# Kernel tuning notes

Measured on AMD Instinct MI355X. Metric: run time of the kernel, lower is better.

The kernel has to match this reference:

```python
import jax, jax.numpy as jnp
from jax import lax
import numpy as np

H, W = 4096, 4096
KERNEL_SIZES = [3, 5, 7, 9, 11, 13, 15]


def setup_inputs() -> dict:
    key = jax.random.key(0)
    k1, k2 = jax.random.split(key)
    x = jax.random.uniform(k1, (H, W), dtype=jnp.float32)
    base_map = jax.random.uniform(k2, (H, W), dtype=jnp.float32)
    return {"x": x, "base_map": base_map}


def _box_blur(x4, k):
    # replicate ('edge') padding by k//2, then VALID conv with uniform 1/k^2 kernel
    p = k // 2
    xp = jnp.pad(x4, ((0, 0), (0, 0), (p, p), (p, p)), mode='edge')
    w = jnp.full((1, 1, k, k), 1.0 / (k * k), dtype=x4.dtype)
    return lax.conv_general_dilated(
        xp, w, window_strides=(1, 1), padding='VALID',
        dimension_numbers=('NCHW', 'OIHW', 'NCHW'))


def reference(x, base_map):
    # x: [H, W] -> [1, 1, H, W]
    x4 = x[None, None, :, :]
    acc = jnp.zeros_like(x4)
    for k in KERNEL_SIZES:  # fixed small set of structurally distinct convs
        acc = acc + _box_blur(x4, k)
    out = (acc / len(KERNEL_SIZES)) * base_map[None, None, :, :]
    return out  # [1, 1, H, W]
```

## Files before the change

### kernel.cpp

```cpp
#include <hip/hip_runtime.h>

typedef __attribute__((ext_vector_type(2))) float f32x2;

#define W 4096
#define H 4096
#define NT 256
#define COLS 512
#define SR 32
#define GROUP 4
#define NSTAGE (SR + 14)
#define NG 12
#define LW 576
#define RAD 7
#define PEND 18

__device__ __forceinline__ void gl_lds16(float* lds, const float* g) {
    __builtin_amdgcn_global_load_lds(
        (const __attribute__((address_space(1))) void*)g,
        (__attribute__((address_space(3))) void*)lds, 16, 0, 0);
}
__device__ __forceinline__ void gl_lds4(float* lds, const float* g) {
    __builtin_amdgcn_global_load_lds(
        (const __attribute__((address_space(1))) void*)g,
        (__attribute__((address_space(3))) void*)lds, 4, 0, 0);
}

__global__ __launch_bounds__(NT, 4) void multibox_kernel(
    const float* __restrict__ x, const float* __restrict__ base,
    float* __restrict__ out)
{
    __shared__ float buf[3][GROUP][LW];

    const int t  = threadIdx.x;
    const int w  = t >> 6;
    const int l  = t & 63;
    const int c0 = blockIdx.x * COLS;
    const int i0 = blockIdx.y * SR;

    const float w3  = 1.f/(7.f*9.f);
    const float w5  = 1.f/(7.f*25.f);
    const float w7  = 1.f/(7.f*49.f);
    const float w9  = 1.f/(7.f*81.f);
    const float w11 = 1.f/(7.f*121.f);
    const float w13 = 1.f/(7.f*169.f);
    const float w15 = 1.f/(7.f*225.f);

    const int colL  = min(max(c0 -   8 +     l, 0), W - 1);
    const int colM1 =         c0 +  56 + 4 * l;
    const int colM2 =         c0 + 312 + 4 * l;
    const int colR  = min(    c0 + 504 +     l,     W - 1);

    auto stage = [&](int g, int b) {
        const int rc = min(max(i0 - RAD + g * GROUP + w, 0), H - 1);
        const float* rp = x + (size_t)rc * W;
        float* lb = &buf[b][w][0];
        gl_lds4 (lb,        rp + colL);
        gl_lds16(lb +  64,  rp + colM1);
        if (l < 48) gl_lds16(lb + 320, rp + colM2);
        gl_lds4 (lb + 512,  rp + colR);
    };

    f32x2 Pnd[PEND];
#pragma unroll
    for (int q = 0; q < PEND; ++q) Pnd[q] = f32x2{0.f, 0.f};

    auto compute_group = [&](int b, int g) {
#pragma unroll
        for (int rr = 0; rr < GROUP; ++rr) {
            if (g * GROUP + rr < NSTAGE) {
                const float* p = &buf[b][rr][2 * t];
                f32x2 q2[9];
#pragma unroll
                for (int i = 0; i < 9; ++i) q2[i] = *(const f32x2*)(p + 2 * i);

                auto PR = [&](int a) -> f32x2 {
                    if ((a & 1) == 0) return q2[a / 2];
                    f32x2 r;
                    r.x = q2[a / 2].y;
                    r.y = q2[a / 2 + 1].x;
                    return r;
                };

                f32x2 s3  = PR(7) + PR(8) + PR(9);
                f32x2 s5  = s3  + PR(6) + PR(10);
                f32x2 s7  = s5  + PR(5) + PR(11);
                f32x2 s9  = s7  + PR(4) + PR(12);
                f32x2 s11 = s9  + PR(3) + PR(13);
                f32x2 s13 = s11 + PR(2) + PR(14);
                f32x2 s15 = s13 + PR(1) + PR(15);

                f32x2 c7 = f32x2{w15, w15} * s15;
                f32x2 c6 = c7 + f32x2{w13, w13} * s13;
                f32x2 c5 = c6 + f32x2{w11, w11} * s11;
                f32x2 c4 = c5 + f32x2{w9 , w9 } * s9;
                f32x2 c3 = c4 + f32x2{w7 , w7 } * s7;
                f32x2 c2 = c3 + f32x2{w5 , w5 } * s5;
                f32x2 c1 = c2 + f32x2{w3 , w3 } * s3;

                Pnd[rr +  0] += c7; Pnd[rr +  1] += c6; Pnd[rr +  2] += c5;
                Pnd[rr +  3] += c4; Pnd[rr +  4] += c3; Pnd[rr +  5] += c2;
                Pnd[rr +  6] += c1; Pnd[rr +  7] += c1; Pnd[rr +  8] += c1;
                Pnd[rr +  9] += c2; Pnd[rr + 10] += c3; Pnd[rr + 11] += c4;
                Pnd[rr + 12] += c5; Pnd[rr + 13] += c6; Pnd[rr + 14] += c7;
            }
        }

#pragma unroll
        for (int p = 0; p < GROUP; ++p) {
            const int o_ofs = 4 * g - 14 + p;
            if (o_ofs >= 0 && o_ofs < SR) {
                const size_t bi = (size_t)(i0 + o_ofs) * W + c0 + 2 * t;
                f32x2 bm = *(const f32x2*)(base + bi);
                f32x2 ov = Pnd[p] * bm;
                *(f32x2*)(out + bi) = ov;
            }
        }

#pragma unroll
        for (int p = 0; p < PEND - GROUP; ++p) Pnd[p] = Pnd[p + GROUP];
#pragma unroll
        for (int p = PEND - GROUP; p < PEND; ++p) Pnd[p] = f32x2{0.f, 0.f};
    };

    stage(0, 0);
    stage(1, 1);
    asm volatile("s_waitcnt vmcnt(4)" ::: "memory");
    __builtin_amdgcn_s_barrier();
    __builtin_amdgcn_sched_barrier(0);

    int b = 0;
#pragma clang loop unroll(disable)
    for (int g = 0; g < NG; ++g) {
        compute_group(b, g);
        int b2 = b + 2; if (b2 >= 3) b2 -= 3;
        if (g + 2 < NG) stage(g + 2, b2);
        if (g + 1 < NG) {
            asm volatile("s_waitcnt vmcnt(4)" ::: "memory");
            __builtin_amdgcn_s_barrier();
            __builtin_amdgcn_sched_barrier(0);
        }
        ++b; if (b >= 3) b = 0;
    }
}

extern "C" void kernel_launch(void* const* d_in, const int* in_sizes, int n_in,
                              void* d_out, int out_size, void* d_ws, size_t ws_size,
                              hipStream_t stream) {
    const float* x    = (const float*)d_in[0];
    const float* base = (const float*)d_in[1];
    float* out        = (float*)d_out;

    dim3 grid(W / COLS, H / SR);
    multibox_kernel<<<grid, dim3(NT), 0, stream>>>(x, base, out);
}
```

Baseline: 46.76 us.

## Make each wave own an independent column strip to drop block barriers

Each wavefront now handles its own 128-column by 32-row tile and keeps a private triple-buffered LDS ring. That removes the workgroup-wide s_barrier, so waves only wait on their own vmcnt counters, and the prefetch is issued before compute in each iteration. The cost is a larger halo: 16 extra columns for every 128 instead of every 512, which means more redundant global loads. It also relies on hand-tuned vmcnt values that must exactly match the number of issued loads, or the wait is wrong.

```diff
diff --git a/kernel.cpp b/kernel.cpp
--- a/kernel.cpp
+++ b/kernel.cpp
@@ -5,12 +5,13 @@
 #define W 4096
 #define H 4096
 #define NT 256
-#define COLS 512
+#define NW 4
+#define WCOLS 128
 #define SR 32
 #define GROUP 4
 #define NSTAGE (SR + 14)
 #define NG 12
-#define LW 576
+#define LW 144
 #define RAD 7
 #define PEND 18
 
@@ -29,13 +30,13 @@
     const float* __restrict__ x, const float* __restrict__ base,
     float* __restrict__ out)
 {
-    __shared__ float buf[3][GROUP][LW];
+    __shared__ float buf[NW][3][GROUP][LW];
 
     const int t  = threadIdx.x;
     const int w  = t >> 6;
     const int l  = t & 63;
-    const int c0 = blockIdx.x * COLS;
-    const int i0 = blockIdx.y * SR;
+    const int cw = blockIdx.x * WCOLS;
+    const int i0 = (blockIdx.y * NW + w) * SR;
 
     const float w3  = 1.f/(7.f*9.f);
     const float w5  = 1.f/(7.f*25.f);
@@ -45,19 +46,22 @@
     const float w13 = 1.f/(7.f*169.f);
     const float w15 = 1.f/(7.f*225.f);
 
-    const int colL  = min(max(c0 -   8 +     l, 0), W - 1);
-    const int colM1 =         c0 +  56 + 4 * l;
-    const int colM2 =         c0 + 312 + 4 * l;
-    const int colR  = min(    c0 + 504 +     l,     W - 1);
+    const int colL = min(max(cw -  8 +     l, 0), W - 1);
+    const int colM =         cw + 56 + 4 * l;
+    const int colR = min(    cw + 120 +    l,     W - 1);
 
     auto stage = [&](int g, int b) {
-        const int rc = min(max(i0 - RAD + g * GROUP + w, 0), H - 1);
-        const float* rp = x + (size_t)rc * W;
-        float* lb = &buf[b][w][0];
-        gl_lds4 (lb,        rp + colL);
-        gl_lds16(lb +  64,  rp + colM1);
-        if (l < 48) gl_lds16(lb + 320, rp + colM2);
-        gl_lds4 (lb + 512,  rp + colR);
+#pragma unroll
+        for (int rr = 0; rr < GROUP; ++rr) {
+            const int rc = min(max(i0 - RAD + g * GROUP + rr, 0), H - 1);
+            const float* rp = x + (size_t)rc * W;
+            float* lb = &buf[w][b][rr][0];
+            gl_lds4(lb, rp + colL);
+            if (l < 16) {
+                gl_lds16(lb +  64, rp + colM);
+                gl_lds4 (lb + 128, rp + colR);
+            }
+        }
     };
 
     f32x2 Pnd[PEND];
@@ -68,7 +72,7 @@
 #pragma unroll
         for (int rr = 0; rr < GROUP; ++rr) {
             if (g * GROUP + rr < NSTAGE) {
-                const float* p = &buf[b][rr][2 * t];
+                const float* p = &buf[w][b][rr][2 * l];
                 f32x2 q2[9];
 #pragma unroll
                 for (int i = 0; i < 9; ++i) q2[i] = *(const f32x2*)(p + 2 * i);
@@ -109,7 +113,7 @@
         for (int p = 0; p < GROUP; ++p) {
             const int o_ofs = 4 * g - 14 + p;
             if (o_ofs >= 0 && o_ofs < SR) {
-                const size_t bi = (size_t)(i0 + o_ofs) * W + c0 + 2 * t;
+                const size_t bi = (size_t)(i0 + o_ofs) * W + cw + 2 * l;
                 f32x2 bm = *(const f32x2*)(base + bi);
                 f32x2 ov = Pnd[p] * bm;
                 *(f32x2*)(out + bi) = ov;
@@ -124,19 +128,21 @@
 
     stage(0, 0);
     stage(1, 1);
-    asm volatile("s_waitcnt vmcnt(4)" ::: "memory");
-    __builtin_amdgcn_s_barrier();
+    asm volatile("s_waitcnt vmcnt(12)" ::: "memory");
     __builtin_amdgcn_sched_barrier(0);
 
     int b = 0;
 #pragma clang loop unroll(disable)
     for (int g = 0; g < NG; ++g) {
-        compute_group(b, g);
         int b2 = b + 2; if (b2 >= 3) b2 -= 3;
         if (g + 2 < NG) stage(g + 2, b2);
+        __builtin_amdgcn_sched_barrier(0);
+        compute_group(b, g);
         if (g + 1 < NG) {
-            asm volatile("s_waitcnt vmcnt(4)" ::: "memory");
-            __builtin_amdgcn_s_barrier();
+            if (g <= 3)          asm volatile("s_waitcnt vmcnt(12)" ::: "memory");
+            else if (g == 4)     asm volatile("s_waitcnt vmcnt(24)" ::: "memory");
+            else if (g == NG - 2)asm volatile("s_waitcnt vmcnt(16)" ::: "memory");
+            else                 asm volatile("s_waitcnt vmcnt(28)" ::: "memory");
             __builtin_amdgcn_sched_barrier(0);
         }
         ++b; if (b >= 3) b = 0;
@@ -150,6 +156,6 @@
     const float* base = (const float*)d_in[1];
     float* out        = (float*)d_out;
 
-    dim3 grid(W / COLS, H / SR);
+    dim3 grid(W / WCOLS, H / (NW * SR));
     multibox_kernel<<<grid, dim3(NT), 0, stream>>>(x, base, out);
 }
```

New measurement: 54.63 us. +16.8%, slower.
